# Optimization experiments

Measured on AMD Instinct MI355X. Metric: run time of the kernel, lower is better.

Reference implementation:

```python
import jax, jax.numpy as jnp
import numpy as np

B, CH, CW, H, FH, FW = 32, 16, 16, 8, 4, 4
NQ = 64
NK = CH * FH * CW * FW  # 4096
D_IN, D_V, D_MODEL = 512, 64, 512


def setup_inputs() -> dict:
    key = jax.random.key(0)
    k1, k2, k3, k4, k5 = jax.random.split(key, 5)
    att12 = jax.random.uniform(k1, (B, CH, CW, H, FH, FW), dtype=jnp.float32)
    att3 = jax.random.uniform(k2, (B, H, NQ, CH * CW), dtype=jnp.float32)
    values = jax.random.normal(k3, (B, NK, D_IN), dtype=jnp.float32)
    # Learned params (xavier-ish scale)
    W_v = jax.random.normal(k4, (H * D_V, D_IN), dtype=jnp.float32) * (1.0 / np.sqrt(D_IN))
    b_v = jnp.zeros((H * D_V,), dtype=jnp.float32)
    W_o = jax.random.normal(k5, (D_MODEL, H * D_V), dtype=jnp.float32) * (1.0 / np.sqrt(H * D_V))
    b_o = jnp.zeros((D_MODEL,), dtype=jnp.float32)
    return {"att12": att12, "att3": att3, "values": values,
            "W_v": W_v, "b_v": b_v, "W_o": W_o, "b_o": b_o}


def reference(att12, att3, values, W_v, b_v, W_o, b_o):
    b_s, h, nq, _ = att3.shape
    ch = cw = CH
    fh, fw = att12.shape[-2:]
    nk = values.shape[1]
    d_v = W_v.shape[0] // h
    # v: [b, h, nk, d_v]
    v = (values @ W_v.T + b_v).reshape(b_s, nk, h, d_v).transpose(0, 2, 1, 3)
    # att12 -> [b, h, 1, ch, cw, fh, fw]
    a12 = jnp.transpose(att12, (0, 3, 1, 2, 4, 5))[:, :, None]
    # att3 -> [b, h, nq, ch, cw, 1, 1]
    a3 = att3.reshape(b_s, h, nq, ch, cw, 1, 1)
    # broadcast multiply, then interleave to key order (ch, fh, cw, fw)
    att = (a12 * a3).transpose(0, 1, 2, 3, 5, 4, 6).reshape(b_s, h, nq, nk)
    att = jax.nn.softmax(att, axis=-1)
    out = jnp.einsum('bhqk,bhkd->bhqd', att, v)
    out = out.transpose(0, 2, 1, 3).reshape(b_s, nq, h * d_v)
    return out @ W_o.T + b_o
```

## Files before the change

kernel.cpp:

```cpp
#include <hip/hip_runtime.h>

typedef short bf16x8 __attribute__((ext_vector_type(8)));
typedef short bf16x4 __attribute__((ext_vector_type(4)));
typedef float f32x4 __attribute__((ext_vector_type(4)));
typedef unsigned int u32x2 __attribute__((ext_vector_type(2)));
typedef unsigned int u32x4 __attribute__((ext_vector_type(4)));

__device__ __forceinline__ unsigned short f2bf(float f) {
  union { float f; unsigned u; } v; v.f = f;
  unsigned r = v.u + 0x7fffu + ((v.u >> 16) & 1u);
  return (unsigned short)(r >> 16);
}

__device__ __forceinline__ unsigned int pk2(float a, float b) {
  union { float f; unsigned u; } x, y; x.f = a; y.f = b;
  return __builtin_amdgcn_perm(y.u + 0x8000u, x.u + 0x8000u, 0x07060302u);
}

__device__ __forceinline__ void gld_lds16(const void* g, void* l) {
  __builtin_amdgcn_global_load_lds(
      (const __attribute__((address_space(1))) void*)g,
      (__attribute__((address_space(3))) void*)l, 16, 0, 0);
}

__global__ __launch_bounds__(256) void prep(const float* __restrict__ W_v,
                                            const float* __restrict__ W_o,
                                            const float* __restrict__ b_v,
                                            const float* __restrict__ b_o,
                                            unsigned short* __restrict__ Wvb,
                                            unsigned short* __restrict__ Wob,
                                            float* __restrict__ bias2) {
  int bid = blockIdx.x;
  if (bid < 512) {
    const float* in = (bid < 256) ? W_v : W_o;
    unsigned short* out = (bid < 256) ? Wvb : Wob;
    long i = (long)((bid & 255) * 256 + threadIdx.x) * 4;
    f32x4 d = *(const f32x4*)(in + i);
    u32x2 w; w[0] = pk2(d[0], d[1]); w[1] = pk2(d[2], d[3]);
    *(u32x2*)(out + i) = w;
  } else {
    int e = (bid - 512) * 256 + threadIdx.x;
    const float* wrow = W_o + (long)e * 512;
    float s = 0.f;
#pragma unroll 4
    for (int d = 0; d < 512; d += 4) {
      f32x4 w = *(const f32x4*)(wrow + d);
      f32x4 bv = *(const f32x4*)(b_v + d);
      s += w[0] * bv[0] + w[1] * bv[1] + w[2] * bv[2] + w[3] * bv[3];
    }
    bias2[e] = s + b_o[e];
  }
}

__global__ __launch_bounds__(256, 2) void vt_gemm(
    const unsigned short* __restrict__ Wvb, const float* __restrict__ V,
    unsigned short* __restrict__ vT) {
  const int t = threadIdx.x, lane = t & 63, wave = t >> 6;
  const int n0 = blockIdx.x * 128;
  const int m0 = blockIdx.y * 128;
  const int b = blockIdx.z;
  const float* Vb = V + (long)b * (4096L * 512) + (long)n0 * 512;

  __shared__ __align__(16) unsigned short As[2][128 * 32];
  __shared__ __align__(16) unsigned short Bs[2][128 * 32];

  const int wm = (wave >> 1) * 64, wn = (wave & 1) * 64;
  const int l16 = lane & 15, quad = lane >> 4;
  const int brow0 = t >> 3, bc4 = (t & 7) * 4;

  f32x4 breg[4];
  auto loadB = [&](int k0) {
#pragma unroll
    for (int j = 0; j < 4; ++j)
      breg[j] = *(const f32x4*)(Vb + (long)(brow0 + 32 * j) * 512 + k0 + bc4);
  };
  auto asyncA = [&](int k0, int buf) {
#pragma unroll
    for (int s = 0; s < 2; ++s) {
      int li = s * 256 + t;
      int row = li >> 2, kq = (li & 3) * 8;
      gld_lds16(Wvb + (long)(m0 + row) * 512 + k0 + kq,
                (char*)&As[buf][0] + (s * 256 + wave * 64) * 16);
    }
  };

  f32x4 acc[4][4];
#pragma unroll
  for (int i = 0; i < 4; ++i)
#pragma unroll
    for (int j = 0; j < 4; ++j) acc[i][j] = (f32x4){0.f, 0.f, 0.f, 0.f};

  asyncA(0, 0);
  loadB(0);

  for (int r = 0; r < 16; ++r) {
    const int buf = r & 1;
#pragma unroll
    for (int j = 0; j < 4; ++j) {
      u32x2 w;
      w[0] = pk2(breg[j][0], breg[j][1]);
      w[1] = pk2(breg[j][2], breg[j][3]);
      *(u32x2*)(&Bs[buf][(brow0 + 32 * j) * 32 + bc4]) = w;
    }
    __syncthreads();
    if (r < 15) {
      loadB((r + 1) * 32);
      asyncA((r + 1) * 32, buf ^ 1);
    }
    bf16x8 af[4], bfv[4];
#pragma unroll
    for (int i = 0; i < 4; ++i)
      af[i] = *(const bf16x8*)(&As[buf][(wm + i * 16 + l16) * 32 + quad * 8]);
#pragma unroll
    for (int j = 0; j < 4; ++j)
      bfv[j] = *(const bf16x8*)(&Bs[buf][(wn + j * 16 + l16) * 32 + quad * 8]);
#pragma unroll
    for (int i = 0; i < 4; ++i)
#pragma unroll
      for (int j = 0; j < 4; ++j)
        acc[i][j] = __builtin_amdgcn_mfma_f32_16x16x32_bf16(af[i], bfv[j], acc[i][j], 0, 0, 0);
  }

  unsigned short* o = vT + (long)b * 2097152;
#pragma unroll
  for (int i = 0; i < 4; ++i)
#pragma unroll
    for (int j = 0; j < 4; ++j) {
      int col = n0 + wn + j * 16 + l16;
#pragma unroll
      for (int r = 0; r < 4; ++r) {
        int row = m0 + wm + i * 16 + quad * 4 + r;
        o[(long)row * 4096 + col] = f2bf(acc[i][j][r]);
      }
    }
}

__global__ __launch_bounds__(256, 2) void o_gemm(
    const float* __restrict__ att12, const float* __restrict__ att3,
    const unsigned short* __restrict__ vT, unsigned short* __restrict__ U) {
  const int bh = blockIdx.x;
  const int b = bh >> 3, h = bh & 7;
  const int t = threadIdx.x, lane = t & 63, wave = t >> 6;

  __shared__ __align__(16) unsigned short As[2][4 * 64 * 32];
  __shared__ __align__(16) unsigned short Bs[2][4 * 64 * 32];
  __shared__ float Ored[64 * 68];
  __shared__ float Zl[4][64];
  __shared__ float rZa[64];

  const unsigned short* vTb = vT + (long)b * 2097152 + (long)h * 64 * 4096;
  const int gq = t & 63, gw = t >> 6;
  const float* a3row = att3 + ((long)bh * 64 + gq) * 256;
  const float* a12b = att12 + (long)b * 32768 + h * 16;
  const int l16 = lane & 15, quad = lane >> 4;

  f32x4 acc[4][4];
#pragma unroll
  for (int i = 0; i < 4; ++i)
#pragma unroll
    for (int j = 0; j < 4; ++j) acc[i][j] = (f32x4){0.f, 0.f, 0.f, 0.f};
  float zacc = 0.f;

  unsigned int pk[16];
  auto genexp = [&](int r) {
    int kbase = gw * 1024 + r * 32;
    int ch = kbase >> 8, fh = (kbase >> 6) & 3, cw0 = (kbase >> 2) & 15;
    f32x4 y0 = *(const f32x4*)(a3row + ch * 16 + cw0);
    f32x4 y1 = *(const f32x4*)(a3row + ch * 16 + cw0 + 4);
    const float* ap = a12b + ch * 2048 + cw0 * 128 + fh * 4;
#pragma unroll
    for (int cw = 0; cw < 8; ++cw) {
      float y = (cw < 4) ? y0[cw] : y1[cw - 4];
      f32x4 x = *(const f32x4*)(ap + cw * 128);
      float e0 = __expf(x[0] * y), e1 = __expf(x[1] * y);
      float e2 = __expf(x[2] * y), e3 = __expf(x[3] * y);
      zacc += (e0 + e1) + (e2 + e3);
      pk[cw * 2] = pk2(e0, e1);
      pk[cw * 2 + 1] = pk2(e2, e3);
    }
  };
  auto asyncB = [&](int r, int buf) {
#pragma unroll
    for (int s = 0; s < 4; ++s) {
      int row = t >> 2, kq = (t & 3) * 8;
      int kk = s * 1024 + r * 32 + kq;
      gld_lds16(vTb + (long)row * 4096 + kk, (char*)&Bs[buf][0] + s * 4096 + wave * 1024);
    }
  };

  asyncB(0, 0);
  genexp(0);

  for (int r = 0; r < 32; ++r) {
    const int buf = r & 1;
    {
      unsigned short* dst = &As[buf][gw * 2048 + gq * 32];
#pragma unroll
      for (int g = 0; g < 4; ++g)
        *(u32x4*)(dst + g * 8) = (u32x4){pk[g * 4], pk[g * 4 + 1], pk[g * 4 + 2], pk[g * 4 + 3]};
    }
    __syncthreads();
    if (r < 31) asyncB(r + 1, buf ^ 1);
    bf16x8 af[4], bfv[4];
#pragma unroll
    for (int i = 0; i < 4; ++i)
      af[i] = *(const bf16x8*)(&As[buf][wave * 2048 + (i * 16 + l16) * 32 + quad * 8]);
#pragma unroll
    for (int j = 0; j < 4; ++j)
      bfv[j] = *(const bf16x8*)(&Bs[buf][wave * 2048 + (j * 16 + l16) * 32 + quad * 8]);
#pragma unroll
    for (int i = 0; i < 4; ++i)
#pragma unroll
      for (int j = 0; j < 4; ++j)
        acc[i][j] = __builtin_amdgcn_mfma_f32_16x16x32_bf16(af[i], bfv[j], acc[i][j], 0, 0, 0);
    if (r < 31) genexp(r + 1);
  }

  Zl[gw][gq] = zacc;
  __syncthreads();
  if (t < 64) rZa[t] = 1.0f / (Zl[0][t] + Zl[1][t] + Zl[2][t] + Zl[3][t]);
#pragma unroll
  for (int w = 0; w < 4; ++w) {
    if (wave == w) {
#pragma unroll
      for (int i = 0; i < 4; ++i)
#pragma unroll
        for (int j = 0; j < 4; ++j) {
          int col = j * 16 + l16;
#pragma unroll
          for (int rr = 0; rr < 4; ++rr) {
            int row = i * 16 + quad * 4 + rr;
            if (w == 0) Ored[row * 68 + col] = acc[i][j][rr];
            else Ored[row * 68 + col] += acc[i][j][rr];
          }
        }
    }
    __syncthreads();
  }
  {
    int q = t >> 2, dv0 = (t & 3) * 16;
    float rz = rZa[q];
    unsigned short* up = U + ((long)(b * 64 + q)) * 512 + h * 64 + dv0;
    u32x4 o0, o1;
#pragma unroll
    for (int j = 0; j < 4; ++j)
      o0[j] = pk2(Ored[q * 68 + dv0 + 2 * j] * rz, Ored[q * 68 + dv0 + 2 * j + 1] * rz);
#pragma unroll
    for (int j = 0; j < 4; ++j)
      o1[j] = pk2(Ored[q * 68 + dv0 + 8 + 2 * j] * rz, Ored[q * 68 + dv0 + 9 + 2 * j] * rz);
    *(u32x4*)(up) = o0;
    *(u32x4*)(up + 8) = o1;
  }
}

template <int BM, int BN>
__global__ __launch_bounds__(256, 2) void gemm_bt(
    const unsigned short* __restrict__ A, const unsigned short* __restrict__ Bt,
    float* __restrict__ C, const float* __restrict__ bias,
    int K, int lda, int ldb, int ldc) {
  constexpr int BK = 32;
  const int t = threadIdx.x;
  const int lane = t & 63;
  const int wave = t >> 6;
  const int m0 = blockIdx.y * BM;
  const int n0 = blockIdx.x * BN;

  A += (long)m0 * lda;
  Bt += (long)n0 * ldb;

  __shared__ __align__(16) unsigned short As[BM * BK];
  __shared__ __align__(16) unsigned short Bs[BN * BK];

  constexpr int TM = BM / 32;
  constexpr int TN = BN / 32;
  const int wm = (wave >> 1) * (BM / 2);
  const int wn = (wave & 1) * (BN / 2);
  const int l16 = lane & 15;
  const int quad = lane >> 4;

  f32x4 acc[TM][TN];
#pragma unroll
  for (int i = 0; i < TM; ++i)
#pragma unroll
    for (int j = 0; j < TN; ++j) acc[i][j] = (f32x4){0.f, 0.f, 0.f, 0.f};

  constexpr int ASHOT = (BM * 4) / 256;
  constexpr int BSHOT = (BN * 4) / 256;

  for (int k0 = 0; k0 < K; k0 += BK) {
#pragma unroll
    for (int s = 0; s < ASHOT; ++s) {
      int li = s * 256 + t;
      int row = li >> 2, kq = (li & 3) * 8;
      gld_lds16(A + (long)row * lda + k0 + kq, (char*)As + (s * 256 + wave * 64) * 16);
    }
#pragma unroll
    for (int s = 0; s < BSHOT; ++s) {
      int li = s * 256 + t;
      int row = li >> 2, kq = (li & 3) * 8;
      gld_lds16(Bt + (long)row * ldb + k0 + kq, (char*)Bs + (s * 256 + wave * 64) * 16);
    }
    __syncthreads();
    bf16x8 af[TM], bfv[TN];
#pragma unroll
    for (int i = 0; i < TM; ++i)
      af[i] = *(const bf16x8*)(As + (wm + i * 16 + l16) * BK + quad * 8);
#pragma unroll
    for (int j = 0; j < TN; ++j)
      bfv[j] = *(const bf16x8*)(Bs + (wn + j * 16 + l16) * BK + quad * 8);
#pragma unroll
    for (int i = 0; i < TM; ++i)
#pragma unroll
      for (int j = 0; j < TN; ++j)
        acc[i][j] = __builtin_amdgcn_mfma_f32_16x16x32_bf16(af[i], bfv[j], acc[i][j], 0, 0, 0);
    __syncthreads();
  }

#pragma unroll
  for (int i = 0; i < TM; ++i) {
#pragma unroll
    for (int j = 0; j < TN; ++j) {
      int col = wn + j * 16 + l16;
#pragma unroll
      for (int r = 0; r < 4; ++r) {
        int row = wm + i * 16 + quad * 4 + r;
        C[(long)(m0 + row) * ldc + (n0 + col)] = acc[i][j][r] + bias[n0 + col];
      }
    }
  }
}

extern "C" void kernel_launch(void* const* d_in, const int* in_sizes, int n_in,
                              void* d_out, int out_size, void* d_ws, size_t ws_size,
                              hipStream_t stream) {
  const float* att12 = (const float*)d_in[0];
  const float* att3  = (const float*)d_in[1];
  const float* values = (const float*)d_in[2];
  const float* W_v = (const float*)d_in[3];
  const float* b_v = (const float*)d_in[4];
  const float* W_o = (const float*)d_in[5];
  const float* b_o = (const float*)d_in[6];
  float* out = (float*)d_out;

  char* ws = (char*)d_ws;
  unsigned short* vT    = (unsigned short*)(ws);
  unsigned short* U     = (unsigned short*)(ws + 134217728L);
  unsigned short* Wvb   = (unsigned short*)(ws + 136314880L);
  unsigned short* Wob   = (unsigned short*)(ws + 136839168L);
  float*          bias2 = (float*)(ws + 137363456L);

  prep<<<dim3(514), dim3(256), 0, stream>>>(W_v, W_o, b_v, b_o, Wvb, Wob, bias2);

  vt_gemm<<<dim3(32, 4, 32), dim3(256), 0, stream>>>(Wvb, values, vT);

  o_gemm<<<dim3(256), dim3(256), 0, stream>>>(att12, att3, vT, U);

  gemm_bt<64, 64><<<dim3(8, 32), dim3(256), 0, stream>>>(
      U, Wob, out, bias2, 512, 512, 512, 512);

  (void)in_sizes; (void)n_in; (void)out_size; (void)ws_size;
}
```

Baseline: 552.3 us.

## Triple-buffer LDS pipelines with manual waitcnt across all three GEMM kernels

Converts the vt_gemm, o_gemm and gemm_bt main loops from single or double buffering to a three-slot LDS ring with a prefetch distance of two. The full __syncthreads is replaced by explicit s_waitcnt vmcnt counts plus s_barrier, so async global-to-LDS loads stay in flight across iterations. o_gemm also pads the A tile row stride to 40 to reduce LDS bank conflicts. This costs more LDS per block, which may reduce occupancy, and relies on hand-tuned vmcnt values being correct. Past the end of K, the prefetch issues redundant loads from offset zero.

```diff
diff --git a/kernel.cpp b/kernel.cpp
--- a/kernel.cpp
+++ b/kernel.cpp
@@ -61,26 +61,28 @@
   const int b = blockIdx.z;
   const float* Vb = V + (long)b * (4096L * 512) + (long)n0 * 512;
 
-  __shared__ __align__(16) unsigned short As[2][128 * 32];
+  __shared__ __align__(16) unsigned short As[3][128 * 32];
   __shared__ __align__(16) unsigned short Bs[2][128 * 32];
 
   const int wm = (wave >> 1) * 64, wn = (wave & 1) * 64;
   const int l16 = lane & 15, quad = lane >> 4;
   const int brow0 = t >> 3, bc4 = (t & 7) * 4;
 
-  f32x4 breg[4];
-  auto loadB = [&](int k0) {
-#pragma unroll
-    for (int j = 0; j < 4; ++j)
-      breg[j] = *(const f32x4*)(Vb + (long)(brow0 + 32 * j) * 512 + k0 + bc4);
-  };
-  auto asyncA = [&](int k0, int buf) {
+  f32x4 breg[2][4];
+  auto loadB = [&](int rr, int bank) {
+    const int k0 = (rr < 16) ? rr * 32 : 0;
+#pragma unroll
+    for (int j = 0; j < 4; ++j)
+      breg[bank][j] = *(const f32x4*)(Vb + (long)(brow0 + 32 * j) * 512 + k0 + bc4);
+  };
+  auto asyncA = [&](int rr, int slot) {
+    const int k0 = (rr < 16) ? rr * 32 : 0;
 #pragma unroll
     for (int s = 0; s < 2; ++s) {
       int li = s * 256 + t;
       int row = li >> 2, kq = (li & 3) * 8;
       gld_lds16(Wvb + (long)(m0 + row) * 512 + k0 + kq,
-                (char*)&As[buf][0] + (s * 256 + wave * 64) * 16);
+                (char*)&As[slot][0] + (s * 256 + wave * 64) * 16);
     }
   };
 
@@ -91,35 +93,42 @@
     for (int j = 0; j < 4; ++j) acc[i][j] = (f32x4){0.f, 0.f, 0.f, 0.f};
 
   asyncA(0, 0);
-  loadB(0);
-
+  loadB(0, 0);
+  asyncA(1, 1);
+  loadB(1, 1);
+
+  int slotR = 0, slotW = 2;
   for (int r = 0; r < 16; ++r) {
-    const int buf = r & 1;
+    const int bank = r & 1;
 #pragma unroll
     for (int j = 0; j < 4; ++j) {
       u32x2 w;
-      w[0] = pk2(breg[j][0], breg[j][1]);
-      w[1] = pk2(breg[j][2], breg[j][3]);
-      *(u32x2*)(&Bs[buf][(brow0 + 32 * j) * 32 + bc4]) = w;
-    }
-    __syncthreads();
-    if (r < 15) {
-      loadB((r + 1) * 32);
-      asyncA((r + 1) * 32, buf ^ 1);
-    }
+      w[0] = pk2(breg[bank][j][0], breg[bank][j][1]);
+      w[1] = pk2(breg[bank][j][2], breg[bank][j][3]);
+      *(u32x2*)(&Bs[bank][(brow0 + 32 * j) * 32 + bc4]) = w;
+    }
+    loadB(r + 2, bank);
+    asm volatile("s_waitcnt vmcnt(10) lgkmcnt(0)" ::: "memory");
+    __builtin_amdgcn_s_barrier();
+    asm volatile("" ::: "memory");
+    asyncA(r + 2, slotW);
+    asm volatile("" ::: "memory");
     bf16x8 af[4], bfv[4];
 #pragma unroll
     for (int i = 0; i < 4; ++i)
-      af[i] = *(const bf16x8*)(&As[buf][(wm + i * 16 + l16) * 32 + quad * 8]);
-#pragma unroll
-    for (int j = 0; j < 4; ++j)
-      bfv[j] = *(const bf16x8*)(&Bs[buf][(wn + j * 16 + l16) * 32 + quad * 8]);
+      af[i] = *(const bf16x8*)(&As[slotR][(wm + i * 16 + l16) * 32 + quad * 8]);
+#pragma unroll
+    for (int j = 0; j < 4; ++j)
+      bfv[j] = *(const bf16x8*)(&Bs[bank][(wn + j * 16 + l16) * 32 + quad * 8]);
 #pragma unroll
     for (int i = 0; i < 4; ++i)
 #pragma unroll
       for (int j = 0; j < 4; ++j)
         acc[i][j] = __builtin_amdgcn_mfma_f32_16x16x32_bf16(af[i], bfv[j], acc[i][j], 0, 0, 0);
-  }
+    slotR = (slotR == 2) ? 0 : slotR + 1;
+    slotW = (slotW == 2) ? 0 : slotW + 1;
+  }
+  asm volatile("s_waitcnt vmcnt(0)" ::: "memory");
 
   unsigned short* o = vT + (long)b * 2097152;
 #pragma unroll
@@ -142,8 +151,8 @@
   const int b = bh >> 3, h = bh & 7;
   const int t = threadIdx.x, lane = t & 63, wave = t >> 6;
 
-  __shared__ __align__(16) unsigned short As[2][4 * 64 * 32];
-  __shared__ __align__(16) unsigned short Bs[2][4 * 64 * 32];
+  __shared__ __align__(16) unsigned short As[2][4 * 64 * 40];
+  __shared__ __align__(16) unsigned short Bs[3][4 * 64 * 32];
   __shared__ float Ored[64 * 68];
   __shared__ float Zl[4][64];
   __shared__ float rZa[64];
@@ -179,42 +188,51 @@
       pk[cw * 2 + 1] = pk2(e2, e3);
     }
   };
-  auto asyncB = [&](int r, int buf) {
+  auto asyncB = [&](int rr, int slot) {
+    const int rc = (rr < 32) ? rr : 0;
 #pragma unroll
     for (int s = 0; s < 4; ++s) {
       int row = t >> 2, kq = (t & 3) * 8;
-      int kk = s * 1024 + r * 32 + kq;
-      gld_lds16(vTb + (long)row * 4096 + kk, (char*)&Bs[buf][0] + s * 4096 + wave * 1024);
+      int kk = s * 1024 + rc * 32 + kq;
+      gld_lds16(vTb + (long)row * 4096 + kk, (char*)&Bs[slot][0] + s * 4096 + wave * 1024);
     }
   };
 
   asyncB(0, 0);
+  asyncB(1, 1);
   genexp(0);
 
+  int slotR = 0, slotW = 2;
   for (int r = 0; r < 32; ++r) {
-    const int buf = r & 1;
+    const int abuf = r & 1;
     {
-      unsigned short* dst = &As[buf][gw * 2048 + gq * 32];
+      unsigned short* dst = &As[abuf][gw * 2560 + gq * 40];
 #pragma unroll
       for (int g = 0; g < 4; ++g)
         *(u32x4*)(dst + g * 8) = (u32x4){pk[g * 4], pk[g * 4 + 1], pk[g * 4 + 2], pk[g * 4 + 3]};
     }
-    __syncthreads();
-    if (r < 31) asyncB(r + 1, buf ^ 1);
+    asm volatile("s_waitcnt vmcnt(4) lgkmcnt(0)" ::: "memory");
+    __builtin_amdgcn_s_barrier();
+    asm volatile("" ::: "memory");
+    asyncB(r + 2, slotW);
+    asm volatile("" ::: "memory");
     bf16x8 af[4], bfv[4];
 #pragma unroll
     for (int i = 0; i < 4; ++i)
-      af[i] = *(const bf16x8*)(&As[buf][wave * 2048 + (i * 16 + l16) * 32 + quad * 8]);
-#pragma unroll
-    for (int j = 0; j < 4; ++j)
-      bfv[j] = *(const bf16x8*)(&Bs[buf][wave * 2048 + (j * 16 + l16) * 32 + quad * 8]);
+      af[i] = *(const bf16x8*)(&As[abuf][wave * 2560 + (i * 16 + l16) * 40 + quad * 8]);
+#pragma unroll
+    for (int j = 0; j < 4; ++j)
+      bfv[j] = *(const bf16x8*)(&Bs[slotR][wave * 2048 + (j * 16 + l16) * 32 + quad * 8]);
 #pragma unroll
     for (int i = 0; i < 4; ++i)
 #pragma unroll
       for (int j = 0; j < 4; ++j)
         acc[i][j] = __builtin_amdgcn_mfma_f32_16x16x32_bf16(af[i], bfv[j], acc[i][j], 0, 0, 0);
     if (r < 31) genexp(r + 1);
-  }
+    slotR = (slotR == 2) ? 0 : slotR + 1;
+    slotW = (slotW == 2) ? 0 : slotW + 1;
+  }
+  asm volatile("s_waitcnt vmcnt(0)" ::: "memory");
 
   Zl[gw][gq] = zacc;
   __syncthreads();
@@ -268,8 +286,8 @@
   A += (long)m0 * lda;
   Bt += (long)n0 * ldb;
 
-  __shared__ __align__(16) unsigned short As[BM * BK];
-  __shared__ __align__(16) unsigned short Bs[BN * BK];
+  __shared__ __align__(16) unsigned short As[3][BM * BK];
+  __shared__ __align__(16) unsigned short Bs[3][BN * BK];
 
   constexpr int TM = BM / 32;
   constexpr int TN = BN / 32;
@@ -286,35 +304,52 @@
 
   constexpr int ASHOT = (BM * 4) / 256;
   constexpr int BSHOT = (BN * 4) / 256;
-
-  for (int k0 = 0; k0 < K; k0 += BK) {
+  const int NIT = K / BK;
+
+  auto stage = [&](int rr, int slot) {
+    const int k0 = ((rr < NIT) ? rr : 0) * BK;
 #pragma unroll
     for (int s = 0; s < ASHOT; ++s) {
       int li = s * 256 + t;
       int row = li >> 2, kq = (li & 3) * 8;
-      gld_lds16(A + (long)row * lda + k0 + kq, (char*)As + (s * 256 + wave * 64) * 16);
+      gld_lds16(A + (long)row * lda + k0 + kq,
+                (char*)&As[slot][0] + (s * 256 + wave * 64) * 16);
     }
 #pragma unroll
     for (int s = 0; s < BSHOT; ++s) {
       int li = s * 256 + t;
       int row = li >> 2, kq = (li & 3) * 8;
-      gld_lds16(Bt + (long)row * ldb + k0 + kq, (char*)Bs + (s * 256 + wave * 64) * 16);
-    }
-    __syncthreads();
+      gld_lds16(Bt + (long)row * ldb + k0 + kq,
+                (char*)&Bs[slot][0] + (s * 256 + wave * 64) * 16);
+    }
+  };
+
+  stage(0, 0);
+  stage(1, 1);
+
+  int slotR = 0, slotW = 2;
+  for (int r = 0; r < NIT; ++r) {
+    asm volatile("s_waitcnt vmcnt(2)" ::: "memory");
+    __builtin_amdgcn_s_barrier();
+    asm volatile("" ::: "memory");
+    stage(r + 2, slotW);
+    asm volatile("" ::: "memory");
     bf16x8 af[TM], bfv[TN];
 #pragma unroll
     for (int i = 0; i < TM; ++i)
-      af[i] = *(const bf16x8*)(As + (wm + i * 16 + l16) * BK + quad * 8);
+      af[i] = *(const bf16x8*)(&As[slotR][(wm + i * 16 + l16) * BK + quad * 8]);
 #pragma unroll
     for (int j = 0; j < TN; ++j)
-      bfv[j] = *(const bf16x8*)(Bs + (wn + j * 16 + l16) * BK + quad * 8);
+      bfv[j] = *(const bf16x8*)(&Bs[slotR][(wn + j * 16 + l16) * BK + quad * 8]);
 #pragma unroll
     for (int i = 0; i < TM; ++i)
 #pragma unroll
       for (int j = 0; j < TN; ++j)
         acc[i][j] = __builtin_amdgcn_mfma_f32_16x16x32_bf16(af[i], bfv[j], acc[i][j], 0, 0, 0);
-    __syncthreads();
-  }
+    slotR = (slotR == 2) ? 0 : slotR + 1;
+    slotW = (slotW == 2) ? 0 : slotW + 1;
+  }
+  asm volatile("s_waitcnt vmcnt(0)" ::: "memory");
 
 #pragma unroll
   for (int i = 0; i < TM; ++i) {
```

Result: no change. 557.2 us (+0.9%).
